# Kernel tuning notes

Hardware: AMD Instinct MI355X
Metric: run time of the kernel (lower is better)

Reference implementation:

```python
import jax, jax.numpy as jnp
import numpy as np


def conv3x3(x, w, b):
    # stride 1, pad 1, NCHW / OIHW
    out = jax.lax.conv_general_dilated(x, w, (1, 1), ((1, 1), (1, 1)),
                                       dimension_numbers=('NCHW', 'OIHW', 'NCHW'))
    return out + b[None, :, None, None]


def bilinear_sample(x, ys, xs):
    # x: [B,C,H,W]; ys,xs: [B,K,H,W] float sampling coords.
    # mmcv-style: zero outside image, per-corner validity.
    B, C, H, W = x.shape
    x_flat = x.reshape(B, C, H * W)
    y0 = jnp.floor(ys)
    x0 = jnp.floor(xs)
    dy = ys - y0
    dx = xs - x0
    y0i = y0.astype(jnp.int32)
    x0i = x0.astype(jnp.int32)

    def corner(yc, xc, wgt):
        valid = (yc >= 0) & (yc < H) & (xc >= 0) & (xc < W)
        idx = jnp.clip(yc, 0, H - 1) * W + jnp.clip(xc, 0, W - 1)  # [B,K,H,W]
        idx_f = idx.reshape(B, -1)
        vals = jax.vmap(lambda xf, ix: xf[:, ix])(x_flat, idx_f)  # [B,C,K*H*W]
        vals = vals.reshape(B, C, *yc.shape[1:])
        return vals * (wgt * valid)[:, None]

    out = corner(y0i, x0i, (1 - dy) * (1 - dx))
    out = out + corner(y0i, x0i + 1, (1 - dy) * dx)
    out = out + corner(y0i + 1, x0i, dy * (1 - dx))
    out = out + corner(y0i + 1, x0i + 1, dy * dx)
    return out  # [B,C,K,H,W]


def avgpool3s2(z):
    # AvgPool2d(kernel=3, stride=2, padding=1), count_include_pad=True -> divide by 9
    s = jax.lax.reduce_window(z, 0.0, jax.lax.add, (1, 1, 3, 3), (1, 1, 2, 2),
                              ((0, 0), (0, 0), (1, 1), (1, 1)))
    return s / 9.0


def setup_inputs() -> dict:
    key = jax.random.key(0)
    k1, k2, k3 = jax.random.split(key, 3)
    C = 64
    x = jax.random.normal(k1, (4, C, 128, 128), dtype=jnp.float32)
    w_off = jax.random.normal(k2, (27, C, 3, 3), dtype=jnp.float32) * 0.02
    b_off = jnp.zeros((27,), dtype=jnp.float32)
    w_align = jax.random.normal(k3, (C, C, 3, 3), dtype=jnp.float32) * 0.02
    b_align = jnp.zeros((C,), dtype=jnp.float32)
    return {"x": x, "w_off": w_off, "b_off": b_off, "w_align": w_align, "b_align": b_align}


def reference(x, w_off, b_off, w_align, b_align):
    B, C, H, W = x.shape
    K = 9
    off_all = conv3x3(x, w_off, b_off)               # [B,27,H,W]
    offset = off_all[:, :2 * K]                      # [B,18,H,W]
    mask = 2.0 * jax.nn.sigmoid(off_all[:, 2 * K:])  # [B,9,H,W]
    off = offset.reshape(B, K, 2, H, W)
    dy = off[:, :, 0]
    dx = off[:, :, 1]
    # base kernel grid (dilation 1, pad 1): offsets in {-1,0,1}
    ky = (jnp.arange(K) // 3 - 1).astype(jnp.float32)
    kx = (jnp.arange(K) % 3 - 1).astype(jnp.float32)
    ys = jnp.arange(H, dtype=jnp.float32)[None, None, :, None] + ky[None, :, None, None] + dy
    xs = jnp.arange(W, dtype=jnp.float32)[None, None, None, :] + kx[None, :, None, None] + dx
    sampled = bilinear_sample(x, ys, xs) * mask[:, None]    # [B,C,K,H,W]
    w = jnp.einsum('bckhw,ock->bohw', sampled, w_align.reshape(C, C, K))
    w = w + b_align[None, :, None, None]
    w = jnp.exp(jax.nn.sigmoid(w))
    return avgpool3s2(w * x) / avgpool3s2(w)
```

## Files before the change

### kernel.cpp

```cpp
#include <hip/hip_runtime.h>
#include <hip/hip_bf16.h>

#define HW 16384
#define CC 64
#define BB 4

typedef __attribute__((ext_vector_type(8))) short bf8;
typedef __attribute__((ext_vector_type(4))) float f4;

static __device__ __forceinline__ unsigned short f2bf(float f) {
    __hip_bfloat16 h = __float2bfloat16(f);
    return *reinterpret_cast<unsigned short*>(&h);
}
static __device__ __forceinline__ float lo16f(unsigned u) { return __uint_as_float(u << 16); }
static __device__ __forceinline__ float hi16f(unsigned u) { return __uint_as_float(u & 0xFFFF0000u); }
static __device__ __forceinline__ unsigned rne_pack(float flo, float fhi) {
    unsigned a = __float_as_uint(flo);
    unsigned b = __float_as_uint(fhi);
    a += 0x7FFFu + ((a >> 16) & 1u);
    b += 0x7FFFu + ((b >> 16) & 1u);
    return __builtin_amdgcn_perm(b, a, 0x07060302u);
}

__global__ __launch_bounds__(256) void k_prep_tx(const float* __restrict__ x,
                                                 const float* __restrict__ w_off,
                                                 const float* __restrict__ w_align,
                                                 unsigned short* __restrict__ xT,
                                                 unsigned short* __restrict__ wA2,
                                                 unsigned short* __restrict__ Wal2) {
    __shared__ unsigned T32[64 * 33];
    int bx = blockIdx.x, t = threadIdx.x;
    if (bx < 216) {
        int i = bx * 256 + t;
        if (i < 32 * 576) {
            int jj = i & 7;
            int chunk = i >> 3;
            int l = chunk & 63;
            int g = chunk >> 6;
            int m2 = g & 1;
            int h2 = (g >> 1) & 1;
            int tp = g >> 2;
            int m = m2 * 16 + (l & 15);
            int c = h2 * 32 + (l >> 4) * 8 + jj;
            float v = (m < 27) ? w_off[m * 576 + c * 9 + tp] : 0.f;
            wA2[i] = f2bf(v);
        } else {
            int j = i - 32 * 576;
            int jj = j & 7;
            int chunk = j >> 3;
            int l = chunk & 63;
            int g = chunk >> 6;
            int mt = g & 3;
            int th = g >> 2;
            int h2 = th & 1;
            int tp = th >> 1;
            int o = mt * 16 + (l & 15);
            int c = h2 * 32 + (l >> 4) * 8 + jj;
            Wal2[j] = f2bf(w_align[o * 576 + c * 9 + tp]);
        }
        return;
    }
    int pix0 = (bx - 216) * 64;
    int b = pix0 >> 14, hw0 = pix0 & (HW - 1);
    const float* xb = x + (size_t)b * CC * HW + hw0;
#pragma unroll
    for (int u = 0; u < 8; u++) {
        int i = t + 256 * u;
        int cp = i >> 6, p = i & 63;
        float v0 = xb[(size_t)(2 * cp) * HW + p];
        float v1 = xb[(size_t)(2 * cp + 1) * HW + p];
        T32[p * 33 + cp] = (unsigned)f2bf(v0) | ((unsigned)f2bf(v1) << 16);
    }
    __syncthreads();
#pragma unroll
    for (int u = 0; u < 2; u++) {
        int i = t + 256 * u;
        int p = i >> 3, q = i & 7;
        uint4 qq;
        qq.x = T32[p * 33 + q * 4 + 0];
        qq.y = T32[p * 33 + q * 4 + 1];
        qq.z = T32[p * 33 + q * 4 + 2];
        qq.w = T32[p * 33 + q * 4 + 3];
        *(uint4*)(xT + ((size_t)b * HW + hw0 + p) * CC + q * 8) = qq;
    }
}

__global__ __launch_bounds__(512, 4) void k_fused(const unsigned short* __restrict__ xT,
                                                  const unsigned short* __restrict__ wA2,
                                                  const unsigned short* __restrict__ Wal2,
                                                  const float* __restrict__ b_off,
                                                  const float* __restrict__ b_align,
                                                  float* __restrict__ wten) {
    __shared__ __align__(16) unsigned short TF[420 * 64];
    __shared__ float OB[27 * 133];

    int t = threadIdx.x, lane = t & 63, wv = t >> 6;
    int quad = lane >> 4, col = lane & 15;
    int bx = blockIdx.x;
    int b = bx >> 7;
    int r = bx & 127;
    int h0 = (r >> 1) * 2;
    int w0 = (r & 1) * 64;
    int pxo = wv * 16 + col;
    int rr = pxo >> 6;
    int hp = h0 + rr, wp = w0 + (pxo & 63);
    int px = (hp << 7) + wp;
    const unsigned short* xTb = xT + (size_t)b * HW * CC;
    const unsigned short* wl = Wal2 + lane * 8;

#pragma unroll
    for (int u = 0; u < 7; u++) {
        int i = t + 512 * u;
        if (i < 3360) {
            int e = i >> 3, s = i & 7;
            int ty = e / 70, tx = e - ty * 70;
            int gy = min(max(h0 - 2 + ty, 0), 127);
            int gx = min(max(w0 - 3 + tx, 0), 127);
            int c = s ^ (e & 7);
            uint4 q = *(const uint4*)(xTb + ((size_t)((gy << 7) + gx)) * CC + c * 8);
            *(uint4*)(TF + i * 8) = q;
        }
    }
    __syncthreads();

    {
        const bf8 zero = {0, 0, 0, 0, 0, 0, 0, 0};
        f4 a0 = {0.f, 0.f, 0.f, 0.f};
        f4 a1 = {0.f, 0.f, 0.f, 0.f};
#pragma unroll
        for (int tap = 0; tap < 9; tap++) {
            int dyt = tap / 3 - 1, dxt = tap - (tap / 3) * 3 - 1;
            int hs = hp + dyt, ws = wp + dxt;
            bool valid = ((unsigned)hs < 128u) && ((unsigned)ws < 128u);
            int e = (rr + dyt + 2) * 70 + (pxo & 63) + dxt + 3;
            int sL = quad ^ (e & 7);
            bf8 b0 = *(const bf8*)(TF + e * 64 + (sL << 3));
            bf8 b1 = *(const bf8*)(TF + e * 64 + ((sL ^ 4) << 3));
            b0 = valid ? b0 : zero;
            b1 = valid ? b1 : zero;
            const bf8 a00 = *(const bf8*)(wA2 + (((tap * 4 + 0) * 64 + lane) << 3));
            const bf8 a01 = *(const bf8*)(wA2 + (((tap * 4 + 1) * 64 + lane) << 3));
            const bf8 a10 = *(const bf8*)(wA2 + (((tap * 4 + 2) * 64 + lane) << 3));
            const bf8 a11 = *(const bf8*)(wA2 + (((tap * 4 + 3) * 64 + lane) << 3));
            a0 = __builtin_amdgcn_mfma_f32_16x16x32_bf16(a00, b0, a0, 0, 0, 0);
            a1 = __builtin_amdgcn_mfma_f32_16x16x32_bf16(a01, b0, a1, 0, 0, 0);
            a0 = __builtin_amdgcn_mfma_f32_16x16x32_bf16(a10, b1, a0, 0, 0, 0);
            a1 = __builtin_amdgcn_mfma_f32_16x16x32_bf16(a11, b1, a1, 0, 0, 0);
        }
#pragma unroll
        for (int i = 0; i < 4; i++) {
            int o0 = quad * 4 + i;
            OB[o0 * 133 + pxo] = a0[i] + b_off[o0];
            int o1 = 16 + o0;
            if (o1 < 27) {
                float v = a1[i] + b_off[o1];
                if (o1 >= 18) v = 2.f / (1.f + __expf(-v));
                OB[o1 * 133 + pxo] = v;
            }
        }
    }

    float dyv[9], dxv[9], mv[9];
#pragma unroll
    for (int k = 0; k < 9; k++) {
        dyv[k] = OB[(2 * k) * 133 + pxo];
        dxv[k] = OB[(2 * k + 1) * 133 + pxo];
        mv[k]  = OB[(18 + k) * 133 + pxo];
    }

    int hm2 = h0 - 2, hp3 = h0 + 3, wm3 = w0 - 3, wp66 = w0 + 66;

    f4 acc[4];
#pragma unroll
    for (int mt = 0; mt < 4; mt++) acc[mt] = (f4){0.f, 0.f, 0.f, 0.f};

#pragma unroll
    for (int k = 0; k < 9; k++) {
        float dy = dyv[k], dx = dxv[k], m = mv[k];
        int k3 = k / 3;
        float ys = (float)(hp + k3 - 1) + dy;
        float xs = (float)(wp + (k - 3 * k3) - 1) + dx;
        float y0f = floorf(ys), x0f = floorf(xs);
        float fy = ys - y0f, fx = xs - x0f;
        int y0 = (int)y0f, x0 = (int)x0f;
        int y1 = y0 + 1, x1 = x0 + 1;
        bool vy0 = (unsigned)y0 < 128u, vy1 = (unsigned)y1 < 128u;
        bool vx0 = (unsigned)x0 < 128u, vx1 = (unsigned)x1 < 128u;
        int cy0 = min(max(y0, 0), 127), cy1 = min(max(y1, 0), 127);
        int cx0 = min(max(x0, 0), 127), cx1 = min(max(x1, 0), 127);
        float w00 = (1.f - fy) * (1.f - fx) * ((vy0 && vx0) ? m : 0.f);
        float w01 = (1.f - fy) * fx         * ((vy0 && vx1) ? m : 0.f);
        float w10 = fy * (1.f - fx)         * ((vy1 && vx0) ? m : 0.f);
        float w11 = fy * fx                 * ((vy1 && vx1) ? m : 0.f);

        bool inT = (cy0 >= hm2) & (cy1 <= hp3) & (cx0 >= wm3) & (cx1 <= wp66);
        uint4 qa0, qa1, qa2, qa3, qb0, qb1, qb2, qb3;
        if (inT) {
            int r0 = (cy0 - hm2) * 70 - wm3, r1 = (cy1 - hm2) * 70 - wm3;
            int e00 = r0 + cx0, e01 = r0 + cx1, e10 = r1 + cx0, e11 = r1 + cx1;
            int s00 = quad ^ (e00 & 7), s01 = quad ^ (e01 & 7);
            int s10 = quad ^ (e10 & 7), s11 = quad ^ (e11 & 7);
            qa0 = *(const uint4*)(TF + e00 * 64 + (s00 << 3));
            qa1 = *(const uint4*)(TF + e01 * 64 + (s01 << 3));
            qa2 = *(const uint4*)(TF + e10 * 64 + (s10 << 3));
            qa3 = *(const uint4*)(TF + e11 * 64 + (s11 << 3));
            qb0 = *(const uint4*)(TF + e00 * 64 + ((s00 ^ 4) << 3));
            qb1 = *(const uint4*)(TF + e01 * 64 + ((s01 ^ 4) << 3));
            qb2 = *(const uint4*)(TF + e10 * 64 + ((s10 ^ 4) << 3));
            qb3 = *(const uint4*)(TF + e11 * 64 + ((s11 ^ 4) << 3));
        } else {
            const unsigned short* c00 = xTb + ((size_t)(cy0 * 128 + cx0)) * CC + quad * 8;
            const unsigned short* c01 = xTb + ((size_t)(cy0 * 128 + cx1)) * CC + quad * 8;
            const unsigned short* c10 = xTb + ((size_t)(cy1 * 128 + cx0)) * CC + quad * 8;
            const unsigned short* c11 = xTb + ((size_t)(cy1 * 128 + cx1)) * CC + quad * 8;
            qa0 = *(const uint4*)(c00);      qa1 = *(const uint4*)(c01);
            qa2 = *(const uint4*)(c10);      qa3 = *(const uint4*)(c11);
            qb0 = *(const uint4*)(c00 + 32); qb1 = *(const uint4*)(c01 + 32);
            qb2 = *(const uint4*)(c10 + 32); qb3 = *(const uint4*)(c11 + 32);
        }

        bf8 bfrag[2];
#pragma unroll
        for (int h2 = 0; h2 < 2; h2++) {
            const unsigned* u0 = (const unsigned*)(h2 ? &qb0 : &qa0);
            const unsigned* u1 = (const unsigned*)(h2 ? &qb1 : &qa1);
            const unsigned* u2 = (const unsigned*)(h2 ? &qb2 : &qa2);
            const unsigned* u3 = (const unsigned*)(h2 ? &qb3 : &qa3);
            __align__(16) unsigned rr4[4];
#pragma unroll
            for (int d = 0; d < 4; d++) {
                unsigned p0 = u0[d], p1 = u1[d], p2 = u2[d], p3 = u3[d];
                float lo = w00 * lo16f(p0) + w01 * lo16f(p1)
                         + w10 * lo16f(p2) + w11 * lo16f(p3);
                float hi = w00 * hi16f(p0) + w01 * hi16f(p1)
                         + w10 * hi16f(p2) + w11 * hi16f(p3);
                rr4[d] = rne_pack(lo, hi);
            }
            bfrag[h2] = *(const bf8*)rr4;
        }
#pragma unroll
        for (int h2 = 0; h2 < 2; h2++) {
#pragma unroll
            for (int mt = 0; mt < 4; mt++) {
                const bf8 a = *(const bf8*)(wl + (size_t)(((k * 2 + h2) * 4 + mt) * 512));
                acc[mt] = __builtin_amdgcn_mfma_f32_16x16x32_bf16(a, bfrag[h2], acc[mt], 0, 0, 0);
            }
        }
    }

    float* wb = wten + (size_t)b * CC * HW + px;
#pragma unroll
    for (int mt = 0; mt < 4; mt++)
#pragma unroll
        for (int i = 0; i < 4; i++) {
            int o = mt * 16 + quad * 4 + i;
            float u = acc[mt][i] + b_align[o];
            float sg = 1.f / (1.f + __expf(-u));
            wb[(size_t)o * HW] = __expf(sg);
        }
}

__global__ __launch_bounds__(256) void k_pool(const float* __restrict__ x,
                                              const float* __restrict__ wten,
                                              float* __restrict__ out) {
    int idx = blockIdx.x * 256 + threadIdx.x;
    int ow = idx & 63;
    int oh = (idx >> 6) & 63;
    int bc = idx >> 12;
    const float* wp = wten + (size_t)bc * HW;
    const float* xp = x + (size_t)bc * HW;
    float num = 0.f, den = 0.f;
#pragma unroll
    for (int iy = 0; iy < 3; iy++) {
        int y = 2 * oh + iy - 1;
        if ((unsigned)y >= 128u) continue;
#pragma unroll
        for (int ix = 0; ix < 3; ix++) {
            int xc = 2 * ow + ix - 1;
            if ((unsigned)xc >= 128u) continue;
            float wv = wp[y * 128 + xc];
            float xv = xp[y * 128 + xc];
            num = fmaf(wv, xv, num);
            den += wv;
        }
    }
    out[idx] = num / den;
}

extern "C" void kernel_launch(void* const* d_in, const int* in_sizes, int n_in,
                              void* d_out, int out_size, void* d_ws, size_t ws_size,
                              hipStream_t stream) {
    const float* x       = (const float*)d_in[0];
    const float* w_off   = (const float*)d_in[1];
    const float* b_off   = (const float*)d_in[2];
    const float* w_align = (const float*)d_in[3];
    const float* b_align = (const float*)d_in[4];
    float* out = (float*)d_out;

    char* p = (char*)d_ws;
    float* wten = (float*)p;                  p += (size_t)BB * CC * HW * 4;
    unsigned short* xT  = (unsigned short*)p; p += (size_t)BB * HW * CC * 2;
    unsigned short* wA2 = (unsigned short*)p; p += 32 * 576 * 2;
    unsigned short* Wal2 = (unsigned short*)p;

    k_prep_tx<<<dim3(1240), dim3(256), 0, stream>>>(x, w_off, w_align, xT, wA2, Wal2);
    k_fused<<<dim3(512), dim3(512), 0, stream>>>(xT, wA2, Wal2, b_off, b_align, wten);
    k_pool<<<dim3(4096), dim3(256), 0, stream>>>(x, wten, out);
}
```

Baseline: 110.8 us.

## Halve fused-kernel block size, each wave handles two pixel rows to reuse weights

The fused deformable-conv kernel now runs 256 threads per block instead of 512. Each wave computes two pixels per lane (upper and lower rows of the 2-row tile), so every weight fragment loaded for the offset conv and the alignment conv feeds two MFMAs. This cuts redundant weight loads per pixel and raises instruction-level parallelism. The cost is more registers per thread (double accumulators) and fewer waves per block, which may lower occupancy or latency hiding.

```diff
diff --git a/kernel.cpp b/kernel.cpp
--- a/kernel.cpp
+++ b/kernel.cpp
@@ -85,7 +85,72 @@
     }
 }
 
-__global__ __launch_bounds__(512, 4) void k_fused(const unsigned short* __restrict__ xT,
+static __device__ __forceinline__ void bilin_px(
+    const unsigned short* __restrict__ TF, const unsigned short* __restrict__ xTb,
+    float dy, float dx, float m, int hp, int wp, int k3, int kx,
+    int hm2, int hp3, int wm3, int wp66, int quad, bf8* bfrag)
+{
+    float ys = (float)(hp + k3 - 1) + dy;
+    float xs = (float)(wp + kx - 1) + dx;
+    float y0f = floorf(ys), x0f = floorf(xs);
+    float fy = ys - y0f, fx = xs - x0f;
+    int y0 = (int)y0f, x0 = (int)x0f;
+    int y1 = y0 + 1, x1 = x0 + 1;
+    bool vy0 = (unsigned)y0 < 128u, vy1 = (unsigned)y1 < 128u;
+    bool vx0 = (unsigned)x0 < 128u, vx1 = (unsigned)x1 < 128u;
+    int cy0 = min(max(y0, 0), 127), cy1 = min(max(y1, 0), 127);
+    int cx0 = min(max(x0, 0), 127), cx1 = min(max(x1, 0), 127);
+    float w00 = (1.f - fy) * (1.f - fx) * ((vy0 && vx0) ? m : 0.f);
+    float w01 = (1.f - fy) * fx         * ((vy0 && vx1) ? m : 0.f);
+    float w10 = fy * (1.f - fx)         * ((vy1 && vx0) ? m : 0.f);
+    float w11 = fy * fx                 * ((vy1 && vx1) ? m : 0.f);
+
+    bool inT = (cy0 >= hm2) & (cy1 <= hp3) & (cx0 >= wm3) & (cx1 <= wp66);
+    uint4 qa0, qa1, qa2, qa3, qb0, qb1, qb2, qb3;
+    if (inT) {
+        int r0 = (cy0 - hm2) * 70 - wm3, r1 = (cy1 - hm2) * 70 - wm3;
+        int e00 = r0 + cx0, e01 = r0 + cx1, e10 = r1 + cx0, e11 = r1 + cx1;
+        int s00 = quad ^ (e00 & 7), s01 = quad ^ (e01 & 7);
+        int s10 = quad ^ (e10 & 7), s11 = quad ^ (e11 & 7);
+        qa0 = *(const uint4*)(TF + e00 * 64 + (s00 << 3));
+        qa1 = *(const uint4*)(TF + e01 * 64 + (s01 << 3));
+        qa2 = *(const uint4*)(TF + e10 * 64 + (s10 << 3));
+        qa3 = *(const uint4*)(TF + e11 * 64 + (s11 << 3));
+        qb0 = *(const uint4*)(TF + e00 * 64 + ((s00 ^ 4) << 3));
+        qb1 = *(const uint4*)(TF + e01 * 64 + ((s01 ^ 4) << 3));
+        qb2 = *(const uint4*)(TF + e10 * 64 + ((s10 ^ 4) << 3));
+        qb3 = *(const uint4*)(TF + e11 * 64 + ((s11 ^ 4) << 3));
+    } else {
+        const unsigned short* c00 = xTb + ((size_t)(cy0 * 128 + cx0)) * CC + quad * 8;
+        const unsigned short* c01 = xTb + ((size_t)(cy0 * 128 + cx1)) * CC + quad * 8;
+        const unsigned short* c10 = xTb + ((size_t)(cy1 * 128 + cx0)) * CC + quad * 8;
+        const unsigned short* c11 = xTb + ((size_t)(cy1 * 128 + cx1)) * CC + quad * 8;
+        qa0 = *(const uint4*)(c00);      qa1 = *(const uint4*)(c01);
+        qa2 = *(const uint4*)(c10);      qa3 = *(const uint4*)(c11);
+        qb0 = *(const uint4*)(c00 + 32); qb1 = *(const uint4*)(c01 + 32);
+        qb2 = *(const uint4*)(c10 + 32); qb3 = *(const uint4*)(c11 + 32);
+    }
+#pragma unroll
+    for (int h2 = 0; h2 < 2; h2++) {
+        const unsigned* u0 = (const unsigned*)(h2 ? &qb0 : &qa0);
+        const unsigned* u1 = (const unsigned*)(h2 ? &qb1 : &qa1);
+        const unsigned* u2 = (const unsigned*)(h2 ? &qb2 : &qa2);
+        const unsigned* u3 = (const unsigned*)(h2 ? &qb3 : &qa3);
+        __align__(16) unsigned rr4[4];
+#pragma unroll
+        for (int d = 0; d < 4; d++) {
+            unsigned p0 = u0[d], p1 = u1[d], p2 = u2[d], p3 = u3[d];
+            float lo = w00 * lo16f(p0) + w01 * lo16f(p1)
+                     + w10 * lo16f(p2) + w11 * lo16f(p3);
+            float hi = w00 * hi16f(p0) + w01 * hi16f(p1)
+                     + w10 * hi16f(p2) + w11 * hi16f(p3);
+            rr4[d] = rne_pack(lo, hi);
+        }
+        bfrag[h2] = *(const bf8*)rr4;
+    }
+}
+
+__global__ __launch_bounds__(256, 2) void k_fused(const unsigned short* __restrict__ xT,
                                                   const unsigned short* __restrict__ wA2,
                                                   const unsigned short* __restrict__ Wal2,
                                                   const float* __restrict__ b_off,
@@ -101,16 +166,16 @@
     int r = bx & 127;
     int h0 = (r >> 1) * 2;
     int w0 = (r & 1) * 64;
-    int pxo = wv * 16 + col;
-    int rr = pxo >> 6;
-    int hp = h0 + rr, wp = w0 + (pxo & 63);
-    int px = (hp << 7) + wp;
+    int pc = wv * 16 + col;
+    int wp = w0 + pc;
+    int pxoL = pc, pxoU = pc + 64;
+    int hL = h0, hU = h0 + 1;
     const unsigned short* xTb = xT + (size_t)b * HW * CC;
     const unsigned short* wl = Wal2 + lane * 8;
 
 #pragma unroll
-    for (int u = 0; u < 7; u++) {
-        int i = t + 512 * u;
+    for (int u = 0; u < 14; u++) {
+        int i = t + 256 * u;
         if (i < 3360) {
             int e = i >> 3, s = i & 7;
             int ty = e / 70, tx = e - ty * 70;
@@ -125,138 +190,99 @@
 
     {
         const bf8 zero = {0, 0, 0, 0, 0, 0, 0, 0};
-        f4 a0 = {0.f, 0.f, 0.f, 0.f};
-        f4 a1 = {0.f, 0.f, 0.f, 0.f};
+        f4 aL0 = {0.f, 0.f, 0.f, 0.f}, aL1 = {0.f, 0.f, 0.f, 0.f};
+        f4 aU0 = {0.f, 0.f, 0.f, 0.f}, aU1 = {0.f, 0.f, 0.f, 0.f};
 #pragma unroll
         for (int tap = 0; tap < 9; tap++) {
             int dyt = tap / 3 - 1, dxt = tap - (tap / 3) * 3 - 1;
-            int hs = hp + dyt, ws = wp + dxt;
-            bool valid = ((unsigned)hs < 128u) && ((unsigned)ws < 128u);
-            int e = (rr + dyt + 2) * 70 + (pxo & 63) + dxt + 3;
-            int sL = quad ^ (e & 7);
-            bf8 b0 = *(const bf8*)(TF + e * 64 + (sL << 3));
-            bf8 b1 = *(const bf8*)(TF + e * 64 + ((sL ^ 4) << 3));
-            b0 = valid ? b0 : zero;
-            b1 = valid ? b1 : zero;
+            int ws = wp + dxt;
+            bool okw = (unsigned)ws < 128u;
+            bool vL = ((unsigned)(hL + dyt) < 128u) && okw;
+            bool vU = ((unsigned)(hU + dyt) < 128u) && okw;
+            int eL = (dyt + 2) * 70 + pc + dxt + 3;
+            int eU = eL + 70;
+            int sLq = quad ^ (eL & 7), sUq = quad ^ (eU & 7);
+            bf8 b0L = *(const bf8*)(TF + eL * 64 + (sLq << 3));
+            bf8 b1L = *(const bf8*)(TF + eL * 64 + ((sLq ^ 4) << 3));
+            bf8 b0U = *(const bf8*)(TF + eU * 64 + (sUq << 3));
+            bf8 b1U = *(const bf8*)(TF + eU * 64 + ((sUq ^ 4) << 3));
+            b0L = vL ? b0L : zero;  b1L = vL ? b1L : zero;
+            b0U = vU ? b0U : zero;  b1U = vU ? b1U : zero;
             const bf8 a00 = *(const bf8*)(wA2 + (((tap * 4 + 0) * 64 + lane) << 3));
             const bf8 a01 = *(const bf8*)(wA2 + (((tap * 4 + 1) * 64 + lane) << 3));
             const bf8 a10 = *(const bf8*)(wA2 + (((tap * 4 + 2) * 64 + lane) << 3));
             const bf8 a11 = *(const bf8*)(wA2 + (((tap * 4 + 3) * 64 + lane) << 3));
-            a0 = __builtin_amdgcn_mfma_f32_16x16x32_bf16(a00, b0, a0, 0, 0, 0);
-            a1 = __builtin_amdgcn_mfma_f32_16x16x32_bf16(a01, b0, a1, 0, 0, 0);
-            a0 = __builtin_amdgcn_mfma_f32_16x16x32_bf16(a10, b1, a0, 0, 0, 0);
-            a1 = __builtin_amdgcn_mfma_f32_16x16x32_bf16(a11, b1, a1, 0, 0, 0);
+            aL0 = __builtin_amdgcn_mfma_f32_16x16x32_bf16(a00, b0L, aL0, 0, 0, 0);
+            aL1 = __builtin_amdgcn_mfma_f32_16x16x32_bf16(a01, b0L, aL1, 0, 0, 0);
+            aL0 = __builtin_amdgcn_mfma_f32_16x16x32_bf16(a10, b1L, aL0, 0, 0, 0);
+            aL1 = __builtin_amdgcn_mfma_f32_16x16x32_bf16(a11, b1L, aL1, 0, 0, 0);
+            aU0 = __builtin_amdgcn_mfma_f32_16x16x32_bf16(a00, b0U, aU0, 0, 0, 0);
+            aU1 = __builtin_amdgcn_mfma_f32_16x16x32_bf16(a01, b0U, aU1, 0, 0, 0);
+            aU0 = __builtin_amdgcn_mfma_f32_16x16x32_bf16(a10, b1U, aU0, 0, 0, 0);
+            aU1 = __builtin_amdgcn_mfma_f32_16x16x32_bf16(a11, b1U, aU1, 0, 0, 0);
         }
 #pragma unroll
         for (int i = 0; i < 4; i++) {
             int o0 = quad * 4 + i;
-            OB[o0 * 133 + pxo] = a0[i] + b_off[o0];
+            OB[o0 * 133 + pxoL] = aL0[i] + b_off[o0];
+            OB[o0 * 133 + pxoU] = aU0[i] + b_off[o0];
             int o1 = 16 + o0;
             if (o1 < 27) {
-                float v = a1[i] + b_off[o1];
-                if (o1 >= 18) v = 2.f / (1.f + __expf(-v));
-                OB[o1 * 133 + pxo] = v;
+                float vL2 = aL1[i] + b_off[o1];
+                float vU2 = aU1[i] + b_off[o1];
+                if (o1 >= 18) {
+                    vL2 = 2.f / (1.f + __expf(-vL2));
+                    vU2 = 2.f / (1.f + __expf(-vU2));
+                }
+                OB[o1 * 133 + pxoL] = vL2;
+                OB[o1 * 133 + pxoU] = vU2;
             }
         }
     }
 
-    float dyv[9], dxv[9], mv[9];
+    int hm2 = h0 - 2, hp3 = h0 + 3, wm3 = w0 - 3, wp66 = w0 + 66;
+
+    f4 accL[4], accU[4];
+#pragma unroll
+    for (int mt = 0; mt < 4; mt++) {
+        accL[mt] = (f4){0.f, 0.f, 0.f, 0.f};
+        accU[mt] = (f4){0.f, 0.f, 0.f, 0.f};
+    }
+
 #pragma unroll
     for (int k = 0; k < 9; k++) {
-        dyv[k] = OB[(2 * k) * 133 + pxo];
-        dxv[k] = OB[(2 * k + 1) * 133 + pxo];
-        mv[k]  = OB[(18 + k) * 133 + pxo];
-    }
-
-    int hm2 = h0 - 2, hp3 = h0 + 3, wm3 = w0 - 3, wp66 = w0 + 66;
-
-    f4 acc[4];
-#pragma unroll
-    for (int mt = 0; mt < 4; mt++) acc[mt] = (f4){0.f, 0.f, 0.f, 0.f};
-
-#pragma unroll
-    for (int k = 0; k < 9; k++) {
-        float dy = dyv[k], dx = dxv[k], m = mv[k];
-        int k3 = k / 3;
-        float ys = (float)(hp + k3 - 1) + dy;
-        float xs = (float)(wp + (k - 3 * k3) - 1) + dx;
-        float y0f = floorf(ys), x0f = floorf(xs);
-        float fy = ys - y0f, fx = xs - x0f;
-        int y0 = (int)y0f, x0 = (int)x0f;
-        int y1 = y0 + 1, x1 = x0 + 1;
-        bool vy0 = (unsigned)y0 < 128u, vy1 = (unsigned)y1 < 128u;
-        bool vx0 = (unsigned)x0 < 128u, vx1 = (unsigned)x1 < 128u;
-        int cy0 = min(max(y0, 0), 127), cy1 = min(max(y1, 0), 127);
-        int cx0 = min(max(x0, 0), 127), cx1 = min(max(x1, 0), 127);
-        float w00 = (1.f - fy) * (1.f - fx) * ((vy0 && vx0) ? m : 0.f);
-        float w01 = (1.f - fy) * fx         * ((vy0 && vx1) ? m : 0.f);
-        float w10 = fy * (1.f - fx)         * ((vy1 && vx0) ? m : 0.f);
-        float w11 = fy * fx                 * ((vy1 && vx1) ? m : 0.f);
-
-        bool inT = (cy0 >= hm2) & (cy1 <= hp3) & (cx0 >= wm3) & (cx1 <= wp66);
-        uint4 qa0, qa1, qa2, qa3, qb0, qb1, qb2, qb3;
-        if (inT) {
-            int r0 = (cy0 - hm2) * 70 - wm3, r1 = (cy1 - hm2) * 70 - wm3;
-            int e00 = r0 + cx0, e01 = r0 + cx1, e10 = r1 + cx0, e11 = r1 + cx1;
-            int s00 = quad ^ (e00 & 7), s01 = quad ^ (e01 & 7);
-            int s10 = quad ^ (e10 & 7), s11 = quad ^ (e11 & 7);
-            qa0 = *(const uint4*)(TF + e00 * 64 + (s00 << 3));
-            qa1 = *(const uint4*)(TF + e01 * 64 + (s01 << 3));
-            qa2 = *(const uint4*)(TF + e10 * 64 + (s10 << 3));
-            qa3 = *(const uint4*)(TF + e11 * 64 + (s11 << 3));
-            qb0 = *(const uint4*)(TF + e00 * 64 + ((s00 ^ 4) << 3));
-            qb1 = *(const uint4*)(TF + e01 * 64 + ((s01 ^ 4) << 3));
-            qb2 = *(const uint4*)(TF + e10 * 64 + ((s10 ^ 4) << 3));
-            qb3 = *(const uint4*)(TF + e11 * 64 + ((s11 ^ 4) << 3));
-        } else {
-            const unsigned short* c00 = xTb + ((size_t)(cy0 * 128 + cx0)) * CC + quad * 8;
-            const unsigned short* c01 = xTb + ((size_t)(cy0 * 128 + cx1)) * CC + quad * 8;
-            const unsigned short* c10 = xTb + ((size_t)(cy1 * 128 + cx0)) * CC + quad * 8;
-            const unsigned short* c11 = xTb + ((size_t)(cy1 * 128 + cx1)) * CC + quad * 8;
-            qa0 = *(const uint4*)(c00);      qa1 = *(const uint4*)(c01);
-            qa2 = *(const uint4*)(c10);      qa3 = *(const uint4*)(c11);
-            qb0 = *(const uint4*)(c00 + 32); qb1 = *(const uint4*)(c01 + 32);
-            qb2 = *(const uint4*)(c10 + 32); qb3 = *(const uint4*)(c11 + 32);
-        }
-
-        bf8 bfrag[2];
-#pragma unroll
-        for (int h2 = 0; h2 < 2; h2++) {
-            const unsigned* u0 = (const unsigned*)(h2 ? &qb0 : &qa0);
-            const unsigned* u1 = (const unsigned*)(h2 ? &qb1 : &qa1);
-            const unsigned* u2 = (const unsigned*)(h2 ? &qb2 : &qa2);
-            const unsigned* u3 = (const unsigned*)(h2 ? &qb3 : &qa3);
-            __align__(16) unsigned rr4[4];
-#pragma unroll
-            for (int d = 0; d < 4; d++) {
-                unsigned p0 = u0[d], p1 = u1[d], p2 = u2[d], p3 = u3[d];
-                float lo = w00 * lo16f(p0) + w01 * lo16f(p1)
-                         + w10 * lo16f(p2) + w11 * lo16f(p3);
-                float hi = w00 * hi16f(p0) + w01 * hi16f(p1)
-                         + w10 * hi16f(p2) + w11 * hi16f(p3);
-                rr4[d] = rne_pack(lo, hi);
-            }
-            bfrag[h2] = *(const bf8*)rr4;
-        }
+        int k3 = k / 3, kx = k - 3 * k3;
+        float dyL = OB[(2 * k) * 133 + pxoL], dxL = OB[(2 * k + 1) * 133 + pxoL];
+        float mL  = OB[(18 + k) * 133 + pxoL];
+        float dyU = OB[(2 * k) * 133 + pxoU], dxU = OB[(2 * k + 1) * 133 + pxoU];
+        float mU  = OB[(18 + k) * 133 + pxoU];
+
+        bf8 bfL[2], bfU[2];
+        bilin_px(TF, xTb, dyL, dxL, mL, hL, wp, k3, kx, hm2, hp3, wm3, wp66, quad, bfL);
+        bilin_px(TF, xTb, dyU, dxU, mU, hU, wp, k3, kx, hm2, hp3, wm3, wp66, quad, bfU);
+
 #pragma unroll
         for (int h2 = 0; h2 < 2; h2++) {
 #pragma unroll
             for (int mt = 0; mt < 4; mt++) {
                 const bf8 a = *(const bf8*)(wl + (size_t)(((k * 2 + h2) * 4 + mt) * 512));
-                acc[mt] = __builtin_amdgcn_mfma_f32_16x16x32_bf16(a, bfrag[h2], acc[mt], 0, 0, 0);
+                accL[mt] = __builtin_amdgcn_mfma_f32_16x16x32_bf16(a, bfL[h2], accL[mt], 0, 0, 0);
+                accU[mt] = __builtin_amdgcn_mfma_f32_16x16x32_bf16(a, bfU[h2], accU[mt], 0, 0, 0);
             }
         }
     }
 
-    float* wb = wten + (size_t)b * CC * HW + px;
+    float* wbL = wten + (size_t)b * CC * HW + (hL << 7) + wp;
+    float* wbU = wten + (size_t)b * CC * HW + (hU << 7) + wp;
 #pragma unroll
     for (int mt = 0; mt < 4; mt++)
 #pragma unroll
         for (int i = 0; i < 4; i++) {
             int o = mt * 16 + quad * 4 + i;
-            float u = acc[mt][i] + b_align[o];
-            float sg = 1.f / (1.f + __expf(-u));
-            wb[(size_t)o * HW] = __expf(sg);
+            float uL = accL[mt][i] + b_align[o];
+            wbL[(size_t)o * HW] = __expf(1.f / (1.f + __expf(-uL)));
+            float uU = accU[mt][i] + b_align[o];
+            wbU[(size_t)o * HW] = __expf(1.f / (1.f + __expf(-uU)));
         }
 }
 
@@ -304,6 +330,6 @@
     unsigned short* Wal2 = (unsigned short*)p;
 
     k_prep_tx<<<dim3(1240), dim3(256), 0, stream>>>(x, w_off, w_align, xT, wA2, Wal2);
-    k_fused<<<dim3(512), dim3(512), 0, stream>>>(xT, wA2, Wal2, b_off, b_align, wten);
+    k_fused<<<dim3(512), dim3(256), 0, stream>>>(xT, wA2, Wal2, b_off, b_align, wten);
     k_pool<<<dim3(4096), dim3(256), 0, stream>>>(x, wten, out);
 }
```

Result: slower. 116.2 us (+4.9%).

## Software-pipeline deformable taps with double-buffered gathers and branchless pointer select

Applied to the files above, without the earlier changes.

The 9-tap deformable sampling loop becomes a two-stage software pipeline. The gathers for tap j+1 are issued before tap j's bilinear mix and MFMAs, using A/B register sets. The LDS-versus-global branch is replaced by a pointer select, so one load path serves both cases, and the second channel half is reached by XOR-ing the address with 64 bytes. Launch bounds are relaxed from 4 to 3 waves per SIMD to make room for the extra registers, trading occupancy for more loads in flight.

```diff
diff --git a/kernel.cpp b/kernel.cpp
--- a/kernel.cpp
+++ b/kernel.cpp
@@ -85,7 +85,77 @@
     }
 }
 
-__global__ __launch_bounds__(512, 4) void k_fused(const unsigned short* __restrict__ xT,
+#define MIXD(P,M) rne_pack( \
+    P##w0*lo16f(P##q0.M)+P##w1*lo16f(P##q1.M)+P##w2*lo16f(P##q2.M)+P##w3*lo16f(P##q3.M), \
+    P##w0*hi16f(P##q0.M)+P##w1*hi16f(P##q1.M)+P##w2*hi16f(P##q2.M)+P##w3*hi16f(P##q3.M))
+#define MIXD2(P,M) rne_pack( \
+    P##w0*lo16f(P##q4.M)+P##w1*lo16f(P##q5.M)+P##w2*lo16f(P##q6.M)+P##w3*lo16f(P##q7.M), \
+    P##w0*hi16f(P##q4.M)+P##w1*hi16f(P##q5.M)+P##w2*hi16f(P##q6.M)+P##w3*hi16f(P##q7.M))
+
+#define PREP(j,P) { \
+    float dy_ = OB[(2*(j))*133+pxo]; \
+    float dx_ = OB[(2*(j)+1)*133+pxo]; \
+    float m_  = OB[(18+(j))*133+pxo]; \
+    const int k3_ = (j)/3, kx_ = (j)-3*k3_; \
+    float ys_ = (float)(hp+k3_-1)+dy_, xs_ = (float)(wp+kx_-1)+dx_; \
+    float y0f_ = floorf(ys_), x0f_ = floorf(xs_); \
+    float fy_ = ys_-y0f_, fx_ = xs_-x0f_; \
+    int y0_ = (int)y0f_, x0_ = (int)x0f_, y1_ = y0_+1, x1_ = x0_+1; \
+    bool vy0_ = (unsigned)y0_<128u, vy1_ = (unsigned)y1_<128u; \
+    bool vx0_ = (unsigned)x0_<128u, vx1_ = (unsigned)x1_<128u; \
+    int cy0_ = min(max(y0_,0),127), cy1_ = min(max(y1_,0),127); \
+    int cx0_ = min(max(x0_,0),127), cx1_ = min(max(x1_,0),127); \
+    P##w0 = (1.f-fy_)*(1.f-fx_)*((vy0_&&vx0_)?m_:0.f); \
+    P##w1 = (1.f-fy_)*fx_      *((vy0_&&vx1_)?m_:0.f); \
+    P##w2 = fy_*(1.f-fx_)      *((vy1_&&vx0_)?m_:0.f); \
+    P##w3 = fy_*fx_            *((vy1_&&vx1_)?m_:0.f); \
+    bool inT_ = (cy0_>=hm2)&(cy1_<=hp3)&(cx0_>=wm3)&(cx1_<=wp66); \
+    int r0_ = (cy0_-hm2)*70-wm3, r1_ = (cy1_-hm2)*70-wm3; \
+    int e00_ = r0_+cx0_, e01_ = r0_+cx1_, e10_ = r1_+cx0_, e11_ = r1_+cx1_; \
+    const unsigned short* p00_ = inT_ ? (TFg + e00_*64 + ((quad^(e00_&7))<<3)) \
+        : xTb + ((size_t)((cy0_<<7)+cx0_))*CC + quad*8; \
+    const unsigned short* p01_ = inT_ ? (TFg + e01_*64 + ((quad^(e01_&7))<<3)) \
+        : xTb + ((size_t)((cy0_<<7)+cx1_))*CC + quad*8; \
+    const unsigned short* p10_ = inT_ ? (TFg + e10_*64 + ((quad^(e10_&7))<<3)) \
+        : xTb + ((size_t)((cy1_<<7)+cx0_))*CC + quad*8; \
+    const unsigned short* p11_ = inT_ ? (TFg + e11_*64 + ((quad^(e11_&7))<<3)) \
+        : xTb + ((size_t)((cy1_<<7)+cx1_))*CC + quad*8; \
+    P##q0 = *(const uint4*)p00_; \
+    P##q1 = *(const uint4*)p01_; \
+    P##q2 = *(const uint4*)p10_; \
+    P##q3 = *(const uint4*)p11_; \
+    P##q4 = *(const uint4*)((unsigned long long)p00_ ^ 64ull); \
+    P##q5 = *(const uint4*)((unsigned long long)p01_ ^ 64ull); \
+    P##q6 = *(const uint4*)((unsigned long long)p10_ ^ 64ull); \
+    P##q7 = *(const uint4*)((unsigned long long)p11_ ^ 64ull); \
+}
+
+#define TAP(j,P) { \
+    uint4 f0_; \
+    f0_.x = MIXD(P,x); f0_.y = MIXD(P,y); f0_.z = MIXD(P,z); f0_.w = MIXD(P,w); \
+    uint4 f1_; \
+    f1_.x = MIXD2(P,x); f1_.y = MIXD2(P,y); f1_.z = MIXD2(P,z); f1_.w = MIXD2(P,w); \
+    bf8 bf0_ = *(const bf8*)&f0_; \
+    bf8 bf1_ = *(const bf8*)&f1_; \
+    const bf8 a0_ = *(const bf8*)(wl + (size_t)((((j)*2+0)*4+0)*512)); \
+    const bf8 a1_ = *(const bf8*)(wl + (size_t)((((j)*2+0)*4+1)*512)); \
+    const bf8 a2_ = *(const bf8*)(wl + (size_t)((((j)*2+0)*4+2)*512)); \
+    const bf8 a3_ = *(const bf8*)(wl + (size_t)((((j)*2+0)*4+3)*512)); \
+    acc[0] = __builtin_amdgcn_mfma_f32_16x16x32_bf16(a0_, bf0_, acc[0], 0, 0, 0); \
+    acc[1] = __builtin_amdgcn_mfma_f32_16x16x32_bf16(a1_, bf0_, acc[1], 0, 0, 0); \
+    acc[2] = __builtin_amdgcn_mfma_f32_16x16x32_bf16(a2_, bf0_, acc[2], 0, 0, 0); \
+    acc[3] = __builtin_amdgcn_mfma_f32_16x16x32_bf16(a3_, bf0_, acc[3], 0, 0, 0); \
+    const bf8 a4_ = *(const bf8*)(wl + (size_t)((((j)*2+1)*4+0)*512)); \
+    const bf8 a5_ = *(const bf8*)(wl + (size_t)((((j)*2+1)*4+1)*512)); \
+    const bf8 a6_ = *(const bf8*)(wl + (size_t)((((j)*2+1)*4+2)*512)); \
+    const bf8 a7_ = *(const bf8*)(wl + (size_t)((((j)*2+1)*4+3)*512)); \
+    acc[0] = __builtin_amdgcn_mfma_f32_16x16x32_bf16(a4_, bf1_, acc[0], 0, 0, 0); \
+    acc[1] = __builtin_amdgcn_mfma_f32_16x16x32_bf16(a5_, bf1_, acc[1], 0, 0, 0); \
+    acc[2] = __builtin_amdgcn_mfma_f32_16x16x32_bf16(a6_, bf1_, acc[2], 0, 0, 0); \
+    acc[3] = __builtin_amdgcn_mfma_f32_16x16x32_bf16(a7_, bf1_, acc[3], 0, 0, 0); \
+}
+
+__global__ __launch_bounds__(512, 3) void k_fused(const unsigned short* __restrict__ xT,
                                                   const unsigned short* __restrict__ wA2,
                                                   const unsigned short* __restrict__ Wal2,
                                                   const float* __restrict__ b_off,
@@ -107,6 +177,7 @@
     int px = (hp << 7) + wp;
     const unsigned short* xTb = xT + (size_t)b * HW * CC;
     const unsigned short* wl = Wal2 + lane * 8;
+    const unsigned short* TFg = TF;
 
 #pragma unroll
     for (int u = 0; u < 7; u++) {
@@ -160,93 +231,26 @@
         }
     }
 
-    float dyv[9], dxv[9], mv[9];
-#pragma unroll
-    for (int k = 0; k < 9; k++) {
-        dyv[k] = OB[(2 * k) * 133 + pxo];
-        dxv[k] = OB[(2 * k + 1) * 133 + pxo];
-        mv[k]  = OB[(18 + k) * 133 + pxo];
-    }
-
     int hm2 = h0 - 2, hp3 = h0 + 3, wm3 = w0 - 3, wp66 = w0 + 66;
 
     f4 acc[4];
 #pragma unroll
     for (int mt = 0; mt < 4; mt++) acc[mt] = (f4){0.f, 0.f, 0.f, 0.f};
 
-#pragma unroll
-    for (int k = 0; k < 9; k++) {
-        float dy = dyv[k], dx = dxv[k], m = mv[k];
-        int k3 = k / 3;
-        float ys = (float)(hp + k3 - 1) + dy;
-        float xs = (float)(wp + (k - 3 * k3) - 1) + dx;
-        float y0f = floorf(ys), x0f = floorf(xs);
-        float fy = ys - y0f, fx = xs - x0f;
-        int y0 = (int)y0f, x0 = (int)x0f;
-        int y1 = y0 + 1, x1 = x0 + 1;
-        bool vy0 = (unsigned)y0 < 128u, vy1 = (unsigned)y1 < 128u;
-        bool vx0 = (unsigned)x0 < 128u, vx1 = (unsigned)x1 < 128u;
-        int cy0 = min(max(y0, 0), 127), cy1 = min(max(y1, 0), 127);
-        int cx0 = min(max(x0, 0), 127), cx1 = min(max(x1, 0), 127);
-        float w00 = (1.f - fy) * (1.f - fx) * ((vy0 && vx0) ? m : 0.f);
-        float w01 = (1.f - fy) * fx         * ((vy0 && vx1) ? m : 0.f);
-        float w10 = fy * (1.f - fx)         * ((vy1 && vx0) ? m : 0.f);
-        float w11 = fy * fx                 * ((vy1 && vx1) ? m : 0.f);
-
-        bool inT = (cy0 >= hm2) & (cy1 <= hp3) & (cx0 >= wm3) & (cx1 <= wp66);
-        uint4 qa0, qa1, qa2, qa3, qb0, qb1, qb2, qb3;
-        if (inT) {
-            int r0 = (cy0 - hm2) * 70 - wm3, r1 = (cy1 - hm2) * 70 - wm3;
-            int e00 = r0 + cx0, e01 = r0 + cx1, e10 = r1 + cx0, e11 = r1 + cx1;
-            int s00 = quad ^ (e00 & 7), s01 = quad ^ (e01 & 7);
-            int s10 = quad ^ (e10 & 7), s11 = quad ^ (e11 & 7);
-            qa0 = *(const uint4*)(TF + e00 * 64 + (s00 << 3));
-            qa1 = *(const uint4*)(TF + e01 * 64 + (s01 << 3));
-            qa2 = *(const uint4*)(TF + e10 * 64 + (s10 << 3));
-            qa3 = *(const uint4*)(TF + e11 * 64 + (s11 << 3));
-            qb0 = *(const uint4*)(TF + e00 * 64 + ((s00 ^ 4) << 3));
-            qb1 = *(const uint4*)(TF + e01 * 64 + ((s01 ^ 4) << 3));
-            qb2 = *(const uint4*)(TF + e10 * 64 + ((s10 ^ 4) << 3));
-            qb3 = *(const uint4*)(TF + e11 * 64 + ((s11 ^ 4) << 3));
-        } else {
-            const unsigned short* c00 = xTb + ((size_t)(cy0 * 128 + cx0)) * CC + quad * 8;
-            const unsigned short* c01 = xTb + ((size_t)(cy0 * 128 + cx1)) * CC + quad * 8;
-            const unsigned short* c10 = xTb + ((size_t)(cy1 * 128 + cx0)) * CC + quad * 8;
-            const unsigned short* c11 = xTb + ((size_t)(cy1 * 128 + cx1)) * CC + quad * 8;
-            qa0 = *(const uint4*)(c00);      qa1 = *(const uint4*)(c01);
-            qa2 = *(const uint4*)(c10);      qa3 = *(const uint4*)(c11);
-            qb0 = *(const uint4*)(c00 + 32); qb1 = *(const uint4*)(c01 + 32);
-            qb2 = *(const uint4*)(c10 + 32); qb3 = *(const uint4*)(c11 + 32);
-        }
-
-        bf8 bfrag[2];
-#pragma unroll
-        for (int h2 = 0; h2 < 2; h2++) {
-            const unsigned* u0 = (const unsigned*)(h2 ? &qb0 : &qa0);
-            const unsigned* u1 = (const unsigned*)(h2 ? &qb1 : &qa1);
-            const unsigned* u2 = (const unsigned*)(h2 ? &qb2 : &qa2);
-            const unsigned* u3 = (const unsigned*)(h2 ? &qb3 : &qa3);
-            __align__(16) unsigned rr4[4];
-#pragma unroll
-            for (int d = 0; d < 4; d++) {
-                unsigned p0 = u0[d], p1 = u1[d], p2 = u2[d], p3 = u3[d];
-                float lo = w00 * lo16f(p0) + w01 * lo16f(p1)
-                         + w10 * lo16f(p2) + w11 * lo16f(p3);
-                float hi = w00 * hi16f(p0) + w01 * hi16f(p1)
-                         + w10 * hi16f(p2) + w11 * hi16f(p3);
-                rr4[d] = rne_pack(lo, hi);
-            }
-            bfrag[h2] = *(const bf8*)rr4;
-        }
-#pragma unroll
-        for (int h2 = 0; h2 < 2; h2++) {
-#pragma unroll
-            for (int mt = 0; mt < 4; mt++) {
-                const bf8 a = *(const bf8*)(wl + (size_t)(((k * 2 + h2) * 4 + mt) * 512));
-                acc[mt] = __builtin_amdgcn_mfma_f32_16x16x32_bf16(a, bfrag[h2], acc[mt], 0, 0, 0);
-            }
-        }
-    }
+    uint4 Aq0, Aq1, Aq2, Aq3, Aq4, Aq5, Aq6, Aq7;
+    uint4 Bq0, Bq1, Bq2, Bq3, Bq4, Bq5, Bq6, Bq7;
+    float Aw0, Aw1, Aw2, Aw3, Bw0, Bw1, Bw2, Bw3;
+
+    PREP(0, A);
+    PREP(1, B); TAP(0, A);
+    PREP(2, A); TAP(1, B);
+    PREP(3, B); TAP(2, A);
+    PREP(4, A); TAP(3, B);
+    PREP(5, B); TAP(4, A);
+    PREP(6, A); TAP(5, B);
+    PREP(7, B); TAP(6, A);
+    PREP(8, A); TAP(7, B);
+    TAP(8, A);
 
     float* wb = wten + (size_t)b * CC * HW + px;
 #pragma unroll
```

Result: slower. 117.3 us (+5.9%).
